# Kernel optimization log

Measured on AMD Instinct MI355X. Metric: run time of the kernel, lower is better.

## Reference

```python
import jax, jax.numpy as jnp
import numpy as np

N = 50000      # nodes
E = 800000     # edges (avg degree 16)
D = 128        # node_dim
H = 3          # total_hops
NE = 16        # num edge types
LN_EPS = 1e-3  # keras LayerNormalization default


def setup_inputs() -> dict:
    key = jax.random.key(0)
    ks = jax.random.split(key, 8)
    scale = 1.0 / np.sqrt(D)
    return {
        "x": jax.random.normal(ks[0], (N, D), jnp.float32),
        "src": jax.random.randint(ks[1], (E,), 0, N, jnp.int32),
        "dest": jax.random.randint(ks[2], (E,), 0, N, jnp.int32),
        "classes": jax.random.randint(ks[3], (E,), 0, NE, jnp.int32),
        "W_src": jax.random.normal(ks[4], (H, D, D), jnp.float32) * scale,
        "b_src": jnp.zeros((H, D), jnp.float32),
        "W_dest": jax.random.normal(ks[5], (H, D, D), jnp.float32) * scale,
        "b_dest": jnp.zeros((H, D), jnp.float32),
        "edge_emb": jax.random.normal(ks[6], (H, NE, D), jnp.float32) * 0.02,
        "ln_gamma": jnp.ones((H, D), jnp.float32),
        "ln_beta": jnp.zeros((H, D), jnp.float32),
    }


def _hop(x, src, dest, classes, Ws, bs, Wd, bd, ee, g, b):
    # dense transforms on nodes [N,D], then gather to edges [E,D]
    s = x @ Ws + bs
    t = x @ Wd + bd
    msgs = jax.nn.relu(s[src] + t[dest] + ee[classes])  # [E,D]
    # unsorted_segment_mean: zero for empty segments (TF semantics)
    summ = jax.ops.segment_sum(msgs, dest, num_segments=N)                    # [N,D]
    cnt = jax.ops.segment_sum(jnp.ones((E, 1), x.dtype), dest, num_segments=N)
    mean = jnp.where(cnt > 0, summ / jnp.maximum(cnt, 1.0), 0.0)
    y = mean + x  # residual add
    mu = jnp.mean(y, axis=-1, keepdims=True)
    var = jnp.mean(jnp.square(y - mu), axis=-1, keepdims=True)
    return g * (y - mu) * jax.lax.rsqrt(var + LN_EPS) + b


def reference(x, src, dest, classes, W_src, b_src, W_dest, b_dest, edge_emb, ln_gamma, ln_beta):
    for i in range(H):
        x = _hop(x, src, dest, classes, W_src[i], b_src[i], W_dest[i], b_dest[i],
                 edge_emb[i], ln_gamma[i], ln_beta[i])
    return x
```

## Files before the change

kernel.cpp:

```cpp
#include <hip/hip_runtime.h>

#define D 128
#define NE 16
#define HOPS 3
#define NSUB 4
#define SCAP 24
#define CAP (NSUB * SCAP)
#define CPAD 32

typedef __attribute__((ext_vector_type(8))) __bf16 bf16x8;
typedef __attribute__((ext_vector_type(4))) __bf16 bf16x4;
typedef __attribute__((ext_vector_type(4))) float f32x4;

#define PK_MASK 0x07FFFFFFu
#define PK_SHIFT 27

__global__ __launch_bounds__(256) void prep_kernel(
    const int* __restrict__ src, const int* __restrict__ dest,
    const int* __restrict__ classes, int* __restrict__ cnt,
    unsigned int* __restrict__ raw, int E, int FB,
    const float* __restrict__ Wsrc, const float* __restrict__ Wdst,
    __bf16* __restrict__ WTs, __bf16* __restrict__ WTd, int WB,
    const float* __restrict__ x, __bf16* __restrict__ xb, int n4, int CB) {
  int b = blockIdx.x;
  int tid = threadIdx.x;
  if (b < FB) {
    int e = b * 256 + tid;
    if (e < E) {
      int d = dest[e];
      int sub = e & (NSUB - 1);
      int p = atomicAdd(&cnt[(size_t)d * CPAD + sub * 8], 1);
      if (p < SCAP)
        raw[(size_t)d * CAP + sub * SCAP + p] =
            (unsigned int)src[e] | ((unsigned int)classes[e] << PK_SHIFT);
    }
  } else if (b < FB + WB) {
    int gid = (b - FB) * 256 + tid;
    int h = gid >> 14;
    int rem = gid & 16383;
    int k = rem >> 7, nn = rem & 127;
    size_t o = (size_t)h * 16384 + nn * 128 + k;
    WTs[o] = (__bf16)Wsrc[gid];
    WTd[o] = (__bf16)Wdst[gid];
  } else {
    int i = (b - FB - WB) * 256 + tid;
    if (i < n4) {
      f32x4 v = ((const f32x4*)x)[i];
      bf16x4 o;
      o[0] = (__bf16)v[0]; o[1] = (__bf16)v[1]; o[2] = (__bf16)v[2]; o[3] = (__bf16)v[3];
      ((bf16x4*)xb)[i] = o;
    }
  }
}

__global__ __launch_bounds__(256) void compact_kernel(
    const int* __restrict__ cnt, const unsigned int* __restrict__ raw,
    unsigned int* __restrict__ pk, int* __restrict__ totc, int n) {
  int wave = threadIdx.x >> 6, lane = threadIdx.x & 63;
  int node = blockIdx.x * 4 + wave;
  if (node >= n) return;
  const int* cb = &cnt[(size_t)node * CPAD];
  int c0 = min(cb[0], SCAP), c1 = min(cb[8], SCAP);
  int c2 = min(cb[16], SCAP), c3 = min(cb[24], SCAP);
  int p1 = c0, p2 = c0 + c1, p3 = p2 + c2, tot = p3 + c3;
  if (lane == 0) totc[node] = tot;
  size_t rbase = (size_t)node * CAP;
  for (int j = lane; j < tot; j += 64) {
    int s_ = (j >= p1) + (j >= p2) + (j >= p3);
    int pofs = s_ == 0 ? 0 : (s_ == 1 ? p1 : (s_ == 2 ? p2 : p3));
    pk[rbase + j] = raw[rbase + s_ * SCAP + (j - pofs)];
  }
}

__global__ __launch_bounds__(256) void gemm_dual(const __bf16* __restrict__ xb,
    const __bf16* __restrict__ WTs, const __bf16* __restrict__ WTd,
    const float* __restrict__ bs, const float* __restrict__ bd,
    __bf16* __restrict__ s_b, __bf16* __restrict__ t_b, int n) {
  int w = threadIdx.x >> 6, l = threadIdx.x & 63;
  int l16 = l & 15, q = l >> 4;
  bf16x8 a[2][4];
  #pragma unroll
  for (int rt = 0; rt < 2; ++rt) {
    int rowA = blockIdx.x * 128 + (w + rt * 4) * 16 + l16;
    int rsafe = rowA < n ? rowA : 0;
    #pragma unroll
    for (int ks = 0; ks < 4; ++ks)
      a[rt][ks] = *(const bf16x8*)&xb[(size_t)rsafe * D + ks * 32 + q * 8];
  }
  f32x4 accS[2][8], accT[2][8];
  #pragma unroll
  for (int rt = 0; rt < 2; ++rt)
    #pragma unroll
    for (int n0 = 0; n0 < 8; ++n0) {
      accS[rt][n0] = (f32x4)0.f;
      accT[rt][n0] = (f32x4)0.f;
    }
  #pragma unroll
  for (int n0 = 0; n0 < 8; ++n0) {
    const __bf16* ps = &WTs[(size_t)(n0 * 16 + l16) * D + q * 8];
    const __bf16* pt = &WTd[(size_t)(n0 * 16 + l16) * D + q * 8];
    #pragma unroll
    for (int ks = 0; ks < 4; ++ks) {
      bf16x8 bfs = *(const bf16x8*)(ps + ks * 32);
      bf16x8 bft = *(const bf16x8*)(pt + ks * 32);
      #pragma unroll
      for (int rt = 0; rt < 2; ++rt) {
        accS[rt][n0] = __builtin_amdgcn_mfma_f32_16x16x32_bf16(a[rt][ks], bfs, accS[rt][n0], 0, 0, 0);
        accT[rt][n0] = __builtin_amdgcn_mfma_f32_16x16x32_bf16(a[rt][ks], bft, accT[rt][n0], 0, 0, 0);
      }
    }
  }
  #pragma unroll
  for (int rt = 0; rt < 2; ++rt) {
    int rowD = blockIdx.x * 128 + (w + rt * 4) * 16 + q * 4;
    #pragma unroll
    for (int n0 = 0; n0 < 8; ++n0) {
      int col = n0 * 16 + l16;
      float bS = bs[col], bT = bd[col];
      #pragma unroll
      for (int r = 0; r < 4; ++r) {
        int row = rowD + r;
        if (row < n) {
          s_b[(size_t)row * D + col] = (__bf16)(accS[rt][n0][r] + bS);
          t_b[(size_t)row * D + col] = (__bf16)(accT[rt][n0][r] + bT);
        }
      }
    }
  }
}

__global__ __launch_bounds__(256) void aggregate_kernel(
    const __bf16* __restrict__ s_b, const __bf16* __restrict__ t_b,
    __bf16* xb,
    const int* __restrict__ totc,
    const unsigned int* __restrict__ pk,
    const float* __restrict__ ee, const float* __restrict__ gamma,
    const float* __restrict__ beta, float* __restrict__ xout,
    int write_xb, int n) {
  __shared__ float ee_s[NE * D];
  for (int i = threadIdx.x; i < NE * D; i += 256) ee_s[i] = ee[i];
  __syncthreads();
  int wave = threadIdx.x >> 6;
  int lane = threadIdx.x & 63;
  int node = blockIdx.x * 4 + wave;
  if (node >= n) return;
  int quarter = lane >> 4;
  int l16 = lane & 15;
  int d0 = l16 * 8;
  size_t nbase = (size_t)node * D;
  bf16x8 tvb = *(const bf16x8*)&t_b[nbase + d0];
  float tv[8];
  #pragma unroll
  for (int j = 0; j < 8; ++j) tv[j] = (float)tvb[j];
  bf16x8 xvb = *(const bf16x8*)&xb[nbase + d0];
  float xr[8];
  #pragma unroll
  for (int j = 0; j < 8; ++j) xr[j] = (float)xvb[j];

  int tot = totc[node];
  int base = node * CAP;
  float acc[8] = {0.f, 0.f, 0.f, 0.f, 0.f, 0.f, 0.f, 0.f};

#define EDGE_ACC(V, SV)                                                        \
  {                                                                            \
    const float* ep = &ee_s[((V) >> PK_SHIFT) * D + d0];                       \
    f32x4 ea = *(const f32x4*)ep, eb = *(const f32x4*)(ep + 4);                \
    _Pragma("unroll")                                                          \
    for (int j = 0; j < 8; ++j) {                                              \
      float u = (float)(SV)[j] + tv[j] + (j < 4 ? ea[j] : eb[j - 4]);          \
      acc[j] += fmaxf(u, 0.f);                                                 \
    }                                                                          \
  }

  int j = quarter;
  for (; j + 12 < tot; j += 16) {
    unsigned int v0 = pk[base + j];
    unsigned int v1 = pk[base + j + 4];
    unsigned int v2 = pk[base + j + 8];
    unsigned int v3 = pk[base + j + 12];
    bf16x8 s0 = *(const bf16x8*)&s_b[(size_t)(v0 & PK_MASK) * D + d0];
    bf16x8 s1 = *(const bf16x8*)&s_b[(size_t)(v1 & PK_MASK) * D + d0];
    bf16x8 s2 = *(const bf16x8*)&s_b[(size_t)(v2 & PK_MASK) * D + d0];
    bf16x8 s3 = *(const bf16x8*)&s_b[(size_t)(v3 & PK_MASK) * D + d0];
    EDGE_ACC(v0, s0); EDGE_ACC(v1, s1); EDGE_ACC(v2, s2); EDGE_ACC(v3, s3);
  }
  for (; j < tot; j += 4) {
    unsigned int v0 = pk[base + j];
    bf16x8 s0 = *(const bf16x8*)&s_b[(size_t)(v0 & PK_MASK) * D + d0];
    EDGE_ACC(v0, s0);
  }
#undef EDGE_ACC

  #pragma unroll
  for (int jj = 0; jj < 8; ++jj) {
    acc[jj] += __shfl_xor(acc[jj], 32);
    acc[jj] += __shfl_xor(acc[jj], 16);
  }
  float invc = tot > 0 ? 1.f / (float)tot : 0.f;
  float y[8];
  #pragma unroll
  for (int jj = 0; jj < 8; ++jj)
    y[jj] = acc[jj] * invc + xr[jj];
  float ssum = 0.f;
  #pragma unroll
  for (int jj = 0; jj < 8; ++jj) ssum += y[jj];
  #pragma unroll
  for (int off = 8; off > 0; off >>= 1) ssum += __shfl_xor(ssum, off);
  float mu = ssum * (1.f / (float)D);
  float dv[8], vs = 0.f;
  #pragma unroll
  for (int jj = 0; jj < 8; ++jj) { dv[jj] = y[jj] - mu; vs += dv[jj] * dv[jj]; }
  #pragma unroll
  for (int off = 8; off > 0; off >>= 1) vs += __shfl_xor(vs, off);
  float inv = rsqrtf(vs * (1.f / (float)D) + 1e-3f);
  if (quarter == 0) {
    f32x4 g0 = *(const f32x4*)&gamma[d0];
    f32x4 g1 = *(const f32x4*)&gamma[d0 + 4];
    f32x4 b0 = *(const f32x4*)&beta[d0];
    f32x4 b1 = *(const f32x4*)&beta[d0 + 4];
    float o[8];
    #pragma unroll
    for (int jj = 0; jj < 8; ++jj)
      o[jj] = (jj < 4 ? g0[jj] : g1[jj - 4]) * dv[jj] * inv + (jj < 4 ? b0[jj] : b1[jj - 4]);
    f32x4 o0, o1;
    #pragma unroll
    for (int jj = 0; jj < 4; ++jj) { o0[jj] = o[jj]; o1[jj] = o[jj + 4]; }
    *(f32x4*)&xout[nbase + d0] = o0;
    *(f32x4*)&xout[nbase + d0 + 4] = o1;
    if (write_xb) {
      bf16x8 ob;
      #pragma unroll
      for (int jj = 0; jj < 8; ++jj) ob[jj] = (__bf16)o[jj];
      *(bf16x8*)&xb[nbase + d0] = ob;
    }
  }
}

extern "C" void kernel_launch(void* const* d_in, const int* in_sizes, int n_in,
                              void* d_out, int out_size, void* d_ws, size_t ws_size,
                              hipStream_t stream) {
  const float* x0     = (const float*)d_in[0];
  const int*   src    = (const int*)d_in[1];
  const int*   dest   = (const int*)d_in[2];
  const int*   cls    = (const int*)d_in[3];
  const float* W_src  = (const float*)d_in[4];
  const float* b_src  = (const float*)d_in[5];
  const float* W_dest = (const float*)d_in[6];
  const float* b_dest = (const float*)d_in[7];
  const float* ee     = (const float*)d_in[8];
  const float* ln_g   = (const float*)d_in[9];
  const float* ln_b   = (const float*)d_in[10];
  float* out = (float*)d_out;

  const int N = in_sizes[0] / D;
  const int E = in_sizes[1];

  char* p = (char*)d_ws;
  __bf16* s_b = (__bf16*)p;   p += (size_t)N * D * sizeof(__bf16);
  __bf16* t_b = (__bf16*)p;   p += (size_t)N * D * sizeof(__bf16);
  __bf16* xb  = (__bf16*)p;   p += (size_t)N * D * sizeof(__bf16);
  __bf16* WTs = (__bf16*)p;   p += (size_t)HOPS * D * D * sizeof(__bf16);
  __bf16* WTd = (__bf16*)p;   p += (size_t)HOPS * D * D * sizeof(__bf16);
  int* cntb   = (int*)p;      p += (size_t)N * CPAD * sizeof(int);
  unsigned int* raw = (unsigned int*)p; p += (size_t)N * CAP * sizeof(unsigned int);
  unsigned int* pk  = (unsigned int*)p; p += (size_t)N * CAP * sizeof(unsigned int);
  int* totc   = (int*)p;      p += (size_t)N * sizeof(int);

  hipMemsetAsync(cntb, 0, (size_t)N * CPAD * sizeof(int), stream);

  const int FB = (E + 255) / 256;
  const int WB = (HOPS * D * D) / 256;
  const int n4 = N * D / 4;
  const int CB = (n4 + 255) / 256;
  prep_kernel<<<FB + WB + CB, 256, 0, stream>>>(
      src, dest, cls, cntb, raw, E, FB,
      W_src, W_dest, WTs, WTd, WB,
      x0, xb, n4, CB);

  compact_kernel<<<(N + 3) / 4, 256, 0, stream>>>(cntb, raw, pk, totc, N);

  for (int h = 0; h < HOPS; ++h) {
    gemm_dual<<<(N + 127) / 128, 256, 0, stream>>>(
        xb, WTs + (size_t)h * D * D, WTd + (size_t)h * D * D,
        b_src + (size_t)h * D, b_dest + (size_t)h * D, s_b, t_b, N);
    aggregate_kernel<<<(N + 3) / 4, 256, 0, stream>>>(
        s_b, t_b, xb, totc, pk,
        ee + (size_t)h * NE * D, ln_g + (size_t)h * D, ln_b + (size_t)h * D,
        out, (h < HOPS - 1) ? 1 : 0, N);
  }
}
```

Before: 301.2 us.

## Split dual GEMM across blocks, fuse hop-0 GEMM with edge bucketing, pack bf16 unpack

The dual src/dest GEMM becomes a single-output GEMM, with the two outputs spread across a 2D grid. That doubles the block count and lowers register pressure per block. The hop-0 GEMM now runs in the same launch as the edge-bucketing atomics, so the two overlap. Weight and x conversion moves into a separate earlier kernel. The aggregate kernel unpacks bf16 with shifts and masks on u32 loads and accumulates in float2 vectors, which may allow packed FP32 math. Costs: A tiles are loaded twice per row block, and there is one extra kernel launch.

Measured after the change: 305.6 us. Within noise of the previous version (+1.5%).

```diff
diff --git a/kernel.cpp b/kernel.cpp
--- a/kernel.cpp
+++ b/kernel.cpp
@@ -11,21 +11,97 @@
 typedef __attribute__((ext_vector_type(8))) __bf16 bf16x8;
 typedef __attribute__((ext_vector_type(4))) __bf16 bf16x4;
 typedef __attribute__((ext_vector_type(4))) float f32x4;
+typedef __attribute__((ext_vector_type(2))) float f32x2;
+typedef __attribute__((ext_vector_type(4))) unsigned int u32x4;
 
 #define PK_MASK 0x07FFFFFFu
 #define PK_SHIFT 27
 
-__global__ __launch_bounds__(256) void prep_kernel(
+__global__ __launch_bounds__(256) void prep0_kernel(
+    const float* __restrict__ Wsrc, const float* __restrict__ Wdst,
+    __bf16* __restrict__ WTs, __bf16* __restrict__ WTd, int WB,
+    const float* __restrict__ x, __bf16* __restrict__ xb, int n4) {
+  int b = blockIdx.x;
+  int tid = threadIdx.x;
+  if (b < WB) {
+    int gid = b * 256 + tid;
+    int h = gid >> 14;
+    int rem = gid & 16383;
+    int k = rem >> 7, nn = rem & 127;
+    size_t o = (size_t)h * 16384 + nn * 128 + k;
+    WTs[o] = (__bf16)Wsrc[gid];
+    WTd[o] = (__bf16)Wdst[gid];
+  } else {
+    int i = (b - WB) * 256 + tid;
+    if (i < n4) {
+      f32x4 v = ((const f32x4*)x)[i];
+      bf16x4 o;
+      o[0] = (__bf16)v[0]; o[1] = (__bf16)v[1]; o[2] = (__bf16)v[2]; o[3] = (__bf16)v[3];
+      ((bf16x4*)xb)[i] = o;
+    }
+  }
+}
+
+__device__ __forceinline__ void gemm_block(const __bf16* __restrict__ xb,
+    const __bf16* __restrict__ WT, const float* __restrict__ bias,
+    __bf16* __restrict__ outb, int rowblk, int n) {
+  int w = threadIdx.x >> 6, l = threadIdx.x & 63;
+  int l16 = l & 15, q = l >> 4;
+  bf16x8 a[2][4];
+  #pragma unroll
+  for (int rt = 0; rt < 2; ++rt) {
+    int rowA = rowblk * 128 + (w + rt * 4) * 16 + l16;
+    int rsafe = rowA < n ? rowA : 0;
+    #pragma unroll
+    for (int ks = 0; ks < 4; ++ks)
+      a[rt][ks] = *(const bf16x8*)&xb[(size_t)rsafe * D + ks * 32 + q * 8];
+  }
+  f32x4 acc[2][8];
+  #pragma unroll
+  for (int rt = 0; rt < 2; ++rt)
+    #pragma unroll
+    for (int n0 = 0; n0 < 8; ++n0) acc[rt][n0] = (f32x4)0.f;
+  #pragma unroll
+  for (int n0 = 0; n0 < 8; ++n0) {
+    const __bf16* pb = &WT[(size_t)(n0 * 16 + l16) * D + q * 8];
+    #pragma unroll
+    for (int ks = 0; ks < 4; ++ks) {
+      bf16x8 bf = *(const bf16x8*)(pb + ks * 32);
+      #pragma unroll
+      for (int rt = 0; rt < 2; ++rt)
+        acc[rt][n0] = __builtin_amdgcn_mfma_f32_16x16x32_bf16(a[rt][ks], bf, acc[rt][n0], 0, 0, 0);
+    }
+  }
+  #pragma unroll
+  for (int rt = 0; rt < 2; ++rt) {
+    int rowD = rowblk * 128 + (w + rt * 4) * 16 + q * 4;
+    #pragma unroll
+    for (int n0 = 0; n0 < 8; ++n0) {
+      int col = n0 * 16 + l16;
+      float bv = bias[col];
+      #pragma unroll
+      for (int r = 0; r < 4; ++r) {
+        int row = rowD + r;
+        if (row < n) outb[(size_t)row * D + col] = (__bf16)(acc[rt][n0][r] + bv);
+      }
+    }
+  }
+}
+
+__global__ __launch_bounds__(256) void gemm0_fill_kernel(
+    const __bf16* __restrict__ xb,
+    const __bf16* __restrict__ WTs, const __bf16* __restrict__ WTd,
+    const float* __restrict__ bs, const float* __restrict__ bd,
+    __bf16* __restrict__ s_b, __bf16* __restrict__ t_b, int n, int GB2,
     const int* __restrict__ src, const int* __restrict__ dest,
     const int* __restrict__ classes, int* __restrict__ cnt,
-    unsigned int* __restrict__ raw, int E, int FB,
-    const float* __restrict__ Wsrc, const float* __restrict__ Wdst,
-    __bf16* __restrict__ WTs, __bf16* __restrict__ WTd, int WB,
-    const float* __restrict__ x, __bf16* __restrict__ xb, int n4, int CB) {
+    unsigned int* __restrict__ raw, int E) {
   int b = blockIdx.x;
-  int tid = threadIdx.x;
-  if (b < FB) {
-    int e = b * 256 + tid;
+  if (b < GB2) {
+    if (b & 1) gemm_block(xb, WTd, bd, t_b, b >> 1, n);
+    else       gemm_block(xb, WTs, bs, s_b, b >> 1, n);
+  } else {
+    int e = (b - GB2) * 256 + threadIdx.x;
     if (e < E) {
       int d = dest[e];
       int sub = e & (NSUB - 1);
@@ -34,23 +110,15 @@
         raw[(size_t)d * CAP + sub * SCAP + p] =
             (unsigned int)src[e] | ((unsigned int)classes[e] << PK_SHIFT);
     }
-  } else if (b < FB + WB) {
-    int gid = (b - FB) * 256 + tid;
-    int h = gid >> 14;
-    int rem = gid & 16383;
-    int k = rem >> 7, nn = rem & 127;
-    size_t o = (size_t)h * 16384 + nn * 128 + k;
-    WTs[o] = (__bf16)Wsrc[gid];
-    WTd[o] = (__bf16)Wdst[gid];
-  } else {
-    int i = (b - FB - WB) * 256 + tid;
-    if (i < n4) {
-      f32x4 v = ((const f32x4*)x)[i];
-      bf16x4 o;
-      o[0] = (__bf16)v[0]; o[1] = (__bf16)v[1]; o[2] = (__bf16)v[2]; o[3] = (__bf16)v[3];
-      ((bf16x4*)xb)[i] = o;
-    }
-  }
+  }
+}
+
+__global__ __launch_bounds__(256) void gemm_st(const __bf16* __restrict__ xb,
+    const __bf16* __restrict__ WTs, const __bf16* __restrict__ WTd,
+    const float* __restrict__ bs, const float* __restrict__ bd,
+    __bf16* __restrict__ s_b, __bf16* __restrict__ t_b, int n) {
+  if (blockIdx.y) gemm_block(xb, WTd, bd, t_b, blockIdx.x, n);
+  else            gemm_block(xb, WTs, bs, s_b, blockIdx.x, n);
 }
 
 __global__ __launch_bounds__(256) void compact_kernel(
@@ -69,63 +137,6 @@
     int s_ = (j >= p1) + (j >= p2) + (j >= p3);
     int pofs = s_ == 0 ? 0 : (s_ == 1 ? p1 : (s_ == 2 ? p2 : p3));
     pk[rbase + j] = raw[rbase + s_ * SCAP + (j - pofs)];
-  }
-}
-
-__global__ __launch_bounds__(256) void gemm_dual(const __bf16* __restrict__ xb,
-    const __bf16* __restrict__ WTs, const __bf16* __restrict__ WTd,
-    const float* __restrict__ bs, const float* __restrict__ bd,
-    __bf16* __restrict__ s_b, __bf16* __restrict__ t_b, int n) {
-  int w = threadIdx.x >> 6, l = threadIdx.x & 63;
-  int l16 = l & 15, q = l >> 4;
-  bf16x8 a[2][4];
-  #pragma unroll
-  for (int rt = 0; rt < 2; ++rt) {
-    int rowA = blockIdx.x * 128 + (w + rt * 4) * 16 + l16;
-    int rsafe = rowA < n ? rowA : 0;
-    #pragma unroll
-    for (int ks = 0; ks < 4; ++ks)
-      a[rt][ks] = *(const bf16x8*)&xb[(size_t)rsafe * D + ks * 32 + q * 8];
-  }
-  f32x4 accS[2][8], accT[2][8];
-  #pragma unroll
-  for (int rt = 0; rt < 2; ++rt)
-    #pragma unroll
-    for (int n0 = 0; n0 < 8; ++n0) {
-      accS[rt][n0] = (f32x4)0.f;
-      accT[rt][n0] = (f32x4)0.f;
-    }
-  #pragma unroll
-  for (int n0 = 0; n0 < 8; ++n0) {
-    const __bf16* ps = &WTs[(size_t)(n0 * 16 + l16) * D + q * 8];
-    const __bf16* pt = &WTd[(size_t)(n0 * 16 + l16) * D + q * 8];
-    #pragma unroll
-    for (int ks = 0; ks < 4; ++ks) {
-      bf16x8 bfs = *(const bf16x8*)(ps + ks * 32);
-      bf16x8 bft = *(const bf16x8*)(pt + ks * 32);
-      #pragma unroll
-      for (int rt = 0; rt < 2; ++rt) {
-        accS[rt][n0] = __builtin_amdgcn_mfma_f32_16x16x32_bf16(a[rt][ks], bfs, accS[rt][n0], 0, 0, 0);
-        accT[rt][n0] = __builtin_amdgcn_mfma_f32_16x16x32_bf16(a[rt][ks], bft, accT[rt][n0], 0, 0, 0);
-      }
-    }
-  }
-  #pragma unroll
-  for (int rt = 0; rt < 2; ++rt) {
-    int rowD = blockIdx.x * 128 + (w + rt * 4) * 16 + q * 4;
-    #pragma unroll
-    for (int n0 = 0; n0 < 8; ++n0) {
-      int col = n0 * 16 + l16;
-      float bS = bs[col], bT = bd[col];
-      #pragma unroll
-      for (int r = 0; r < 4; ++r) {
-        int row = rowD + r;
-        if (row < n) {
-          s_b[(size_t)row * D + col] = (__bf16)(accS[rt][n0][r] + bS);
-          t_b[(size_t)row * D + col] = (__bf16)(accT[rt][n0][r] + bT);
-        }
-      }
-    }
   }
 }
 
@@ -149,26 +160,36 @@
   int d0 = l16 * 8;
   size_t nbase = (size_t)node * D;
   bf16x8 tvb = *(const bf16x8*)&t_b[nbase + d0];
-  float tv[8];
-  #pragma unroll
-  for (int j = 0; j < 8; ++j) tv[j] = (float)tvb[j];
+  f32x2 tv2[4];
+  #pragma unroll
+  for (int k = 0; k < 4; ++k) { tv2[k][0] = (float)tvb[2 * k]; tv2[k][1] = (float)tvb[2 * k + 1]; }
   bf16x8 xvb = *(const bf16x8*)&xb[nbase + d0];
-  float xr[8];
-  #pragma unroll
-  for (int j = 0; j < 8; ++j) xr[j] = (float)xvb[j];
 
   int tot = totc[node];
   int base = node * CAP;
-  float acc[8] = {0.f, 0.f, 0.f, 0.f, 0.f, 0.f, 0.f, 0.f};
-
-#define EDGE_ACC(V, SV)                                                        \
+  f32x2 acc2[4];
+  #pragma unroll
+  for (int k = 0; k < 4; ++k) acc2[k] = (f32x2)0.f;
+
+#define EDGE_ACC(V, SU)                                                        \
   {                                                                            \
-    const float* ep = &ee_s[((V) >> PK_SHIFT) * D + d0];                       \
-    f32x4 ea = *(const f32x4*)ep, eb = *(const f32x4*)(ep + 4);                \
+    const float* ep_ = &ee_s[((V) >> PK_SHIFT) * D + d0];                      \
+    f32x4 ea_ = *(const f32x4*)ep_, eb_ = *(const f32x4*)(ep_ + 4);            \
+    f32x2 epr_[4];                                                             \
+    epr_[0][0] = ea_[0]; epr_[0][1] = ea_[1];                                  \
+    epr_[1][0] = ea_[2]; epr_[1][1] = ea_[3];                                  \
+    epr_[2][0] = eb_[0]; epr_[2][1] = eb_[1];                                  \
+    epr_[3][0] = eb_[2]; epr_[3][1] = eb_[3];                                  \
     _Pragma("unroll")                                                          \
-    for (int j = 0; j < 8; ++j) {                                              \
-      float u = (float)(SV)[j] + tv[j] + (j < 4 ? ea[j] : eb[j - 4]);          \
-      acc[j] += fmaxf(u, 0.f);                                                 \
+    for (int k_ = 0; k_ < 4; ++k_) {                                           \
+      unsigned int u_ = (SU)[k_];                                              \
+      f32x2 v_;                                                                \
+      v_[0] = __uint_as_float(u_ << 16);                                       \
+      v_[1] = __uint_as_float(u_ & 0xFFFF0000u);                               \
+      v_ = v_ + tv2[k_] + epr_[k_];                                            \
+      v_[0] = fmaxf(v_[0], 0.f);                                               \
+      v_[1] = fmaxf(v_[1], 0.f);                                               \
+      acc2[k_] += v_;                                                          \
     }                                                                          \
   }
 
@@ -178,29 +199,33 @@
     unsigned int v1 = pk[base + j + 4];
     unsigned int v2 = pk[base + j + 8];
     unsigned int v3 = pk[base + j + 12];
-    bf16x8 s0 = *(const bf16x8*)&s_b[(size_t)(v0 & PK_MASK) * D + d0];
-    bf16x8 s1 = *(const bf16x8*)&s_b[(size_t)(v1 & PK_MASK) * D + d0];
-    bf16x8 s2 = *(const bf16x8*)&s_b[(size_t)(v2 & PK_MASK) * D + d0];
-    bf16x8 s3 = *(const bf16x8*)&s_b[(size_t)(v3 & PK_MASK) * D + d0];
+    u32x4 s0 = *(const u32x4*)&s_b[(size_t)(v0 & PK_MASK) * D + d0];
+    u32x4 s1 = *(const u32x4*)&s_b[(size_t)(v1 & PK_MASK) * D + d0];
+    u32x4 s2 = *(const u32x4*)&s_b[(size_t)(v2 & PK_MASK) * D + d0];
+    u32x4 s3 = *(const u32x4*)&s_b[(size_t)(v3 & PK_MASK) * D + d0];
     EDGE_ACC(v0, s0); EDGE_ACC(v1, s1); EDGE_ACC(v2, s2); EDGE_ACC(v3, s3);
   }
   for (; j < tot; j += 4) {
     unsigned int v0 = pk[base + j];
-    bf16x8 s0 = *(const bf16x8*)&s_b[(size_t)(v0 & PK_MASK) * D + d0];
+    u32x4 s0 = *(const u32x4*)&s_b[(size_t)(v0 & PK_MASK) * D + d0];
     EDGE_ACC(v0, s0);
   }
 #undef EDGE_ACC
 
   #pragma unroll
-  for (int jj = 0; jj < 8; ++jj) {
-    acc[jj] += __shfl_xor(acc[jj], 32);
-    acc[jj] += __shfl_xor(acc[jj], 16);
+  for (int k = 0; k < 4; ++k) {
+    acc2[k][0] += __shfl_xor(acc2[k][0], 32);
+    acc2[k][0] += __shfl_xor(acc2[k][0], 16);
+    acc2[k][1] += __shfl_xor(acc2[k][1], 32);
+    acc2[k][1] += __shfl_xor(acc2[k][1], 16);
   }
   float invc = tot > 0 ? 1.f / (float)tot : 0.f;
   float y[8];
   #pragma unroll
-  for (int jj = 0; jj < 8; ++jj)
-    y[jj] = acc[jj] * invc + xr[jj];
+  for (int k = 0; k < 4; ++k) {
+    y[2 * k]     = acc2[k][0] * invc + (float)xvb[2 * k];
+    y[2 * k + 1] = acc2[k][1] * invc + (float)xvb[2 * k + 1];
+  }
   float ssum = 0.f;
   #pragma unroll
   for (int jj = 0; jj < 8; ++jj) ssum += y[jj];
@@ -268,21 +293,26 @@
 
   hipMemsetAsync(cntb, 0, (size_t)N * CPAD * sizeof(int), stream);
 
-  const int FB = (E + 255) / 256;
   const int WB = (HOPS * D * D) / 256;
   const int n4 = N * D / 4;
   const int CB = (n4 + 255) / 256;
-  prep_kernel<<<FB + WB + CB, 256, 0, stream>>>(
-      src, dest, cls, cntb, raw, E, FB,
-      W_src, W_dest, WTs, WTd, WB,
-      x0, xb, n4, CB);
+  const int FB = (E + 255) / 256;
+  const int GB2 = ((N + 127) / 128) * 2;
+
+  prep0_kernel<<<WB + CB, 256, 0, stream>>>(W_src, W_dest, WTs, WTd, WB, x0, xb, n4);
+
+  gemm0_fill_kernel<<<GB2 + FB, 256, 0, stream>>>(
+      xb, WTs, WTd, b_src, b_dest, s_b, t_b, N, GB2,
+      src, dest, cls, cntb, raw, E);
 
   compact_kernel<<<(N + 3) / 4, 256, 0, stream>>>(cntb, raw, pk, totc, N);
 
   for (int h = 0; h < HOPS; ++h) {
-    gemm_dual<<<(N + 127) / 128, 256, 0, stream>>>(
-        xb, WTs + (size_t)h * D * D, WTd + (size_t)h * D * D,
-        b_src + (size_t)h * D, b_dest + (size_t)h * D, s_b, t_b, N);
+    if (h > 0) {
+      gemm_st<<<dim3((N + 127) / 128, 2), 256, 0, stream>>>(
+          xb, WTs + (size_t)h * D * D, WTd + (size_t)h * D * D,
+          b_src + (size_t)h * D, b_dest + (size_t)h * D, s_b, t_b, N);
+    }
     aggregate_kernel<<<(N + 3) / 4, 256, 0, stream>>>(
         s_b, t_b, xb, totc, pk,
         ee + (size_t)h * NE * D, ln_g + (size_t)h * D, ln_b + (size_t)h * D,
```
